# Optimization experiments

Hardware: AMD Instinct MI355X
Metric: run time of the kernel (lower is better)

The kernel has to match this reference:

```python
import jax, jax.numpy as jnp
import numpy as np

N = 50000          # nodes
E = 1600000        # edges (avg degree 32)
NUM_FEAT = 512
HIDDEN = 128
NUM_CLASS = 40
NUM_LAYERS = 4
EPS = 0.3


def setup_inputs() -> dict:
    key = jax.random.key(0)
    ks = jax.random.split(key, 8)
    x = jax.random.normal(ks[0], (N, NUM_FEAT), dtype=jnp.float32)
    edge_index = jax.random.randint(ks[1], (2, E), 0, N, dtype=jnp.int64)
    gain = 1.414  # xavier_normal_(gain=1.414) as in reset_parameters
    W1 = jax.random.normal(ks[2], (HIDDEN, NUM_FEAT), dtype=jnp.float32) * gain * (2.0 / (HIDDEN + NUM_FEAT)) ** 0.5
    b1 = jnp.zeros((HIDDEN,), dtype=jnp.float32)
    W2 = jax.random.normal(ks[3], (NUM_CLASS, HIDDEN), dtype=jnp.float32) * gain * (2.0 / (NUM_CLASS + HIDDEN)) ** 0.5
    b2 = jnp.zeros((NUM_CLASS,), dtype=jnp.float32)
    # FAConv attention vectors: Linear(channels, 1, bias=False) per layer
    att_l = jax.random.normal(ks[4], (NUM_LAYERS, HIDDEN), dtype=jnp.float32) * (2.0 / (1 + HIDDEN)) ** 0.5
    att_r = jax.random.normal(ks[5], (NUM_LAYERS, HIDDEN), dtype=jnp.float32) * (2.0 / (1 + HIDDEN)) ** 0.5
    return dict(x=x, edge_index=edge_index, W1=W1, b1=b1, W2=W2, b2=b2, att_l=att_l, att_r=att_r)


def reference(x, edge_index, W1, b1, W2, b2, att_l, att_r):
    n = x.shape[0]
    # gcn_norm with self-loops (FAConv default add_self_loops=True)
    loops = jnp.arange(n, dtype=edge_index.dtype)
    src = jnp.concatenate([edge_index[0], loops])  # source j
    dst = jnp.concatenate([edge_index[1], loops])  # target i
    deg = jax.ops.segment_sum(jnp.ones_like(src, dtype=x.dtype), dst, num_segments=n)
    dis = jax.lax.rsqrt(jnp.maximum(deg, 1.0))
    norm = dis[src] * dis[dst]  # [E+N]

    # eval mode: dropout is identity
    h = jax.nn.relu(x @ W1.T + b1)  # [N, HIDDEN]
    raw = h
    for l in range(NUM_LAYERS):
        al = h @ att_l[l]  # [N]
        ar = h @ att_r[l]  # [N]
        coef = jnp.tanh(al[src] + ar[dst]) * norm            # [E+N]
        agg = jax.ops.segment_sum(h[src] * coef[:, None], dst, num_segments=n)
        h = agg + EPS * raw
    logits = h @ W2.T + b2  # [N, NUM_CLASS]
    return jax.nn.log_softmax(logits, axis=1)
```

## Files before the change

kernel.cpp:

```cpp
#include <hip/hip_runtime.h>
#include <cmath>


#define HIDDEN 128
#define FEAT 512
#define NCLASS 40
#define LDST 40
#define LDSW 132
#define NB 256
#define PITCH 12544
#define BM1 64

typedef __attribute__((ext_vector_type(8))) short short8;
typedef __attribute__((ext_vector_type(4))) float f32x4;
typedef __attribute__((ext_vector_type(2))) float f32x2;

__device__ __forceinline__ float bf_lo(unsigned u) { return __uint_as_float(u << 16); }
__device__ __forceinline__ float bf_hi(unsigned u) { return __uint_as_float(u & 0xffff0000u); }
__device__ __forceinline__ f32x2 up2(unsigned u) {
    f32x2 v; v.x = bf_lo(u); v.y = bf_hi(u); return v;
}
__device__ __forceinline__ unsigned pack_bf16(float x, float y) {
    unsigned ux = __float_as_uint(x);
    unsigned uy = __float_as_uint(y);
    unsigned lx = (ux + 0x7fffu + ((ux >> 16) & 1u)) >> 16;
    unsigned hy = (uy + 0x7fffu + ((uy >> 16) & 1u)) & 0xffff0000u;
    return hy | lx;
}
__device__ __forceinline__ float fast_tanh(float x) {
    x = fminf(fmaxf(x, -15.f), 15.f);
    float e = __expf(2.f * x);
    return (e - 1.f) / (e + 1.f);
}

#define ACC4P(c, r) { f32x2 c2; c2.x = c; c2.y = c; \
    acc2[0] = __builtin_elementwise_fma(c2, up2(r.x), acc2[0]); \
    acc2[1] = __builtin_elementwise_fma(c2, up2(r.y), acc2[1]); \
    acc2[2] = __builtin_elementwise_fma(c2, up2(r.z), acc2[2]); \
    acc2[3] = __builtin_elementwise_fma(c2, up2(r.w), acc2[3]); }

__global__ __launch_bounds__(256) void k_hist(const int* __restrict__ ei, int E, int CE,
                                              unsigned* __restrict__ partial,
                                              ushort* __restrict__ lrank) {
    __shared__ unsigned lh[PITCH];
    const int b = blockIdx.x, tid = threadIdx.x;
    for (int w = tid; w < PITCH; w += 256) lh[w] = 0;
    __syncthreads();
    int e0 = b * CE, e1 = min(E, e0 + CE);
    for (int e = e0 + tid; e < e1; e += 256) {
        int dst = ei[E + e];
        int sh = (dst & 3) * 8;
        unsigned old = atomicAdd(&lh[dst >> 2], 1u << sh);
        lrank[e] = (ushort)((old >> sh) & 0xffu);
    }
    __syncthreads();
    unsigned* prow = partial + (size_t)b * PITCH;
    for (int w = tid; w < PITCH; w += 256) prow[w] = lh[w];
}

__global__ __launch_bounds__(256) void k_hscan(unsigned* __restrict__ partial,
                                               int* __restrict__ deg,
                                               float* __restrict__ dis, int n) {
    int w = blockIdx.x * 256 + threadIdx.x;
    if (w >= PITCH) return;
    unsigned run = 0;
    size_t idx = w;
    for (int b = 0; b < NB; ++b, idx += PITCH) {
        unsigned v = partial[idx];
        partial[idx] = run;
        run += v;
    }
    int node = 4 * w;
    int d0 = run & 0xffu, d1 = (run >> 8) & 0xffu, d2 = (run >> 16) & 0xffu, d3 = run >> 24;
    if (node < n)     { deg[node]     = d0; dis[node]     = rsqrtf((float)(d0 + 1)); }
    if (node + 1 < n) { deg[node + 1] = d1; dis[node + 1] = rsqrtf((float)(d1 + 1)); }
    if (node + 2 < n) { deg[node + 2] = d2; dis[node + 2] = rsqrtf((float)(d2 + 1)); }
    if (node + 3 < n) { deg[node + 3] = d3; dis[node + 3] = rsqrtf((float)(d3 + 1)); }
}

__global__ __launch_bounds__(256) void k_scan1(const int* __restrict__ deg, int* __restrict__ offs,
                                               int* __restrict__ part, int n) {
    __shared__ int s[256];
    int tid = threadIdx.x;
    int gid = blockIdx.x * 256 + tid;
    int v = (gid < n) ? deg[gid] : 0;
    s[tid] = v;
    __syncthreads();
    for (int off = 1; off < 256; off <<= 1) {
        int t = (tid >= off) ? s[tid - off] : 0;
        __syncthreads();
        s[tid] += t;
        __syncthreads();
    }
    if (gid < n) offs[gid] = s[tid] - v;
    if (tid == 255) part[blockIdx.x] = s[255];
}

__global__ __launch_bounds__(256) void k_scan2(int* __restrict__ part, int nb) {
    __shared__ int s[256];
    int tid = threadIdx.x;
    int v = (tid < nb) ? part[tid] : 0;
    s[tid] = v;
    __syncthreads();
    for (int off = 1; off < 256; off <<= 1) {
        int t = (tid >= off) ? s[tid - off] : 0;
        __syncthreads();
        s[tid] += t;
        __syncthreads();
    }
    if (tid < nb) part[tid] = s[tid] - v;
}

__global__ __launch_bounds__(256) void k_scan3(int* __restrict__ offs, const int* __restrict__ part,
                                               int n, int E) {
    int gid = blockIdx.x * 256 + threadIdx.x;
    if (gid < n) offs[gid] += part[blockIdx.x];
    if (gid == 0) offs[n] = E;
}

__global__ __launch_bounds__(256) void k_csr_fill(const int* __restrict__ ei, int E, int CE,
                                                  const int* __restrict__ offs,
                                                  const unsigned* __restrict__ partial,
                                                  const ushort* __restrict__ lrank,
                                                  int* __restrict__ csrc) {
    __shared__ unsigned lp[PITCH];
    const int b = blockIdx.x, tid = threadIdx.x;
    const unsigned* prow = partial + (size_t)b * PITCH;
    for (int w = tid; w < PITCH; w += 256) lp[w] = prow[w];
    __syncthreads();
    int e0 = b * CE, e1 = min(E, e0 + CE);
    for (int e = e0 + tid; e < e1; e += 256) {
        int dst = ei[E + e];
        int src = ei[e];
        unsigned wv = lp[dst >> 2];
        int base = (wv >> ((dst & 3) * 8)) & 0xffu;
        csrc[offs[dst] + base + (int)lrank[e]] = src;
    }
}

__global__ __launch_bounds__(256) void k_gemm1p(const float* __restrict__ x,
                                                const float* __restrict__ W1,
                                                const float* __restrict__ b1,
                                                float* __restrict__ h,
                                                unsigned* __restrict__ hbf,
                                                const float* __restrict__ attl,
                                                const float* __restrict__ attr,
                                                const float* __restrict__ dis,
                                                float2* __restrict__ al2,
                                                float* __restrict__ ar_out, int M) {
    __shared__ ushort As[BM1 * LDST];
    __shared__ ushort Bs[128 * LDST];
    __shared__ float hs[BM1][HIDDEN + 1];
    const int tid = threadIdx.x;
    const int bm = blockIdx.x * BM1;
    const int wave = tid >> 6, lane = tid & 63;
    const int rh = (wave >> 1) * 32;
    const int ch = (wave & 1) * 64;
    const int sub = lane & 15, quad = lane >> 4;
    const int lrow = tid >> 3;
    const int lcol = (tid & 7) * 4;
    f32x4 acc[2][4] = {};
    float4 av[2], bv[4];
#pragma unroll
    for (int i = 0; i < 2; ++i) {
        int grow = bm + lrow + 32 * i;
        av[i] = (grow < M) ? *(const float4*)(x + (size_t)grow * FEAT + lcol)
                           : make_float4(0.f, 0.f, 0.f, 0.f);
    }
#pragma unroll
    for (int i = 0; i < 4; ++i)
        bv[i] = *(const float4*)(W1 + (size_t)(lrow + 32 * i) * FEAT + lcol);

    for (int k0 = 0; k0 < FEAT; k0 += 32) {
#pragma unroll
        for (int i = 0; i < 2; ++i)
            *(uint2*)(As + (lrow + 32 * i) * LDST + lcol) =
                make_uint2(pack_bf16(av[i].x, av[i].y), pack_bf16(av[i].z, av[i].w));
#pragma unroll
        for (int i = 0; i < 4; ++i)
            *(uint2*)(Bs + (lrow + 32 * i) * LDST + lcol) =
                make_uint2(pack_bf16(bv[i].x, bv[i].y), pack_bf16(bv[i].z, bv[i].w));
        __syncthreads();
        if (k0 + 32 < FEAT) {
            const int kn = k0 + 32;
#pragma unroll
            for (int i = 0; i < 2; ++i) {
                int grow = bm + lrow + 32 * i;
                av[i] = (grow < M) ? *(const float4*)(x + (size_t)grow * FEAT + kn + lcol)
                                   : make_float4(0.f, 0.f, 0.f, 0.f);
            }
#pragma unroll
            for (int i = 0; i < 4; ++i)
                bv[i] = *(const float4*)(W1 + (size_t)(lrow + 32 * i) * FEAT + kn + lcol);
        }
        short8 af[2], bfr[4];
#pragma unroll
        for (int t = 0; t < 2; ++t)
            af[t] = *(const short8*)(As + (rh + t * 16 + sub) * LDST + quad * 8);
#pragma unroll
        for (int u = 0; u < 4; ++u)
            bfr[u] = *(const short8*)(Bs + (ch + u * 16 + sub) * LDST + quad * 8);
#pragma unroll
        for (int t = 0; t < 2; ++t)
#pragma unroll
            for (int u = 0; u < 4; ++u)
                acc[t][u] = __builtin_amdgcn_mfma_f32_16x16x32_bf16(af[t], bfr[u], acc[t][u], 0, 0, 0);
        __syncthreads();
    }
    float b1v[4];
#pragma unroll
    for (int u = 0; u < 4; ++u) b1v[u] = b1[ch + u * 16 + sub];
#pragma unroll
    for (int t = 0; t < 2; ++t) {
#pragma unroll
        for (int u = 0; u < 4; ++u) {
            int col = ch + u * 16 + sub;
#pragma unroll
            for (int r2 = 0; r2 < 4; ++r2) {
                int r = rh + t * 16 + quad * 4 + r2;
                int grow = bm + r;
                float v = fmaxf(acc[t][u][r2] + b1v[u], 0.f);
                hs[r][col] = v;
                if (grow < M)
                    h[(size_t)grow * HIDDEN + col] = v;
            }
        }
    }
    __syncthreads();
    {
        const float al0 = attl[2 * lane], al1 = attl[2 * lane + 1];
        const float ab0 = attr[2 * lane], ab1 = attr[2 * lane + 1];
        for (int i = 0; i < 16; ++i) {
            int ln = wave * 16 + i;
            int node = bm + ln;
            if (node >= M) break;
            float2 hv = *(const float2*)(&hs[ln][2 * lane]);
            hbf[(size_t)node * 64 + lane] = pack_bf16(hv.x, hv.y);
            float pl = hv.x * al0 + hv.y * al1;
            float pr = hv.x * ab0 + hv.y * ab1;
            for (int off = 32; off; off >>= 1) {
                pl += __shfl_down(pl, off);
                pr += __shfl_down(pr, off);
            }
            if (lane == 0) {
                al2[node] = make_float2(pl, dis[node]);
                ar_out[node] = pr;
            }
        }
    }
}

__global__ __launch_bounds__(256) void k_aggregate(
                            const unsigned* __restrict__ hbf, const float* __restrict__ raw,
                            const float2* __restrict__ al2, const float* __restrict__ ar,
                            const int* __restrict__ offs, const int* __restrict__ csrc,
                            float* __restrict__ hout, unsigned* __restrict__ houtbf,
                            const float* __restrict__ attl_n, const float* __restrict__ attr_n,
                            float2* __restrict__ al2_o, float* __restrict__ ar_o, int n) {
    int node = (blockIdx.x * blockDim.x + threadIdx.x) >> 6;
    int lane = threadIdx.x & 63;
    if (node >= n) return;
    const int grp = lane >> 4;
    const int sub = lane & 15;
    const float arn = ar[node];
    const float2 selfld = al2[node];
    const float disn = selfld.y;
    f32x2 acc2[4] = {};
    int e0 = offs[node], e1 = offs[node + 1];
    for (int base = e0; base < e1; base += 64) {
        int cnt = min(64, e1 - base);
        int idx = base + lane;
        int smy = (lane < cnt) ? csrc[idx] : node;
        float2 lmy = al2[smy];
        float cmy = (lane < cnt) ? fast_tanh(lmy.x + arn) * lmy.y * disn : 0.f;
        int t = 0;
        for (; t + 16 <= cnt; t += 16) {
            int sa = __shfl(smy, t + grp);
            int sb = __shfl(smy, t + 4 + grp);
            int sc = __shfl(smy, t + 8 + grp);
            int sd = __shfl(smy, t + 12 + grp);
            float ca = __shfl(cmy, t + grp);
            float cb = __shfl(cmy, t + 4 + grp);
            float cc = __shfl(cmy, t + 8 + grp);
            float cd = __shfl(cmy, t + 12 + grp);
            uint4 ra = *(const uint4*)(hbf + (size_t)sa * 64 + sub * 4);
            uint4 rb = *(const uint4*)(hbf + (size_t)sb * 64 + sub * 4);
            uint4 rc = *(const uint4*)(hbf + (size_t)sc * 64 + sub * 4);
            uint4 rd = *(const uint4*)(hbf + (size_t)sd * 64 + sub * 4);
            ACC4P(ca, ra); ACC4P(cb, rb); ACC4P(cc, rc); ACC4P(cd, rd);
        }
        for (; t < cnt; t += 4) {
            int sa = __shfl(smy, t + grp);
            float ca = __shfl(cmy, t + grp);
            uint4 ra = *(const uint4*)(hbf + (size_t)sa * 64 + sub * 4);
            ACC4P(ca, ra);
        }
    }
#pragma unroll
    for (int j = 0; j < 4; ++j) {
        acc2[j].x += __shfl_xor(acc2[j].x, 16);
        acc2[j].y += __shfl_xor(acc2[j].y, 16);
        acc2[j].x += __shfl_xor(acc2[j].x, 32);
        acc2[j].y += __shfl_xor(acc2[j].y, 32);
    }
    {
        float c = fast_tanh(selfld.x + arn) * disn * disn;
        uint4 r = *(const uint4*)(hbf + (size_t)node * 64 + sub * 4);
        ACC4P(c, r);
    }
    float o[8];
    {
        float4 rv0 = *(const float4*)(raw + (size_t)node * HIDDEN + sub * 8);
        float4 rv1 = *(const float4*)(raw + (size_t)node * HIDDEN + sub * 8 + 4);
        o[0] = acc2[0].x + 0.3f * rv0.x; o[1] = acc2[0].y + 0.3f * rv0.y;
        o[2] = acc2[1].x + 0.3f * rv0.z; o[3] = acc2[1].y + 0.3f * rv0.w;
        o[4] = acc2[2].x + 0.3f * rv1.x; o[5] = acc2[2].y + 0.3f * rv1.y;
        o[6] = acc2[3].x + 0.3f * rv1.z; o[7] = acc2[3].y + 0.3f * rv1.w;
    }
    if (grp == 0) {
        if (hout) {
            *(float4*)(hout + (size_t)node * HIDDEN + sub * 8) = make_float4(o[0], o[1], o[2], o[3]);
            *(float4*)(hout + (size_t)node * HIDDEN + sub * 8 + 4) = make_float4(o[4], o[5], o[6], o[7]);
        }
        if (houtbf) {
            uint4 pk = make_uint4(pack_bf16(o[0], o[1]), pack_bf16(o[2], o[3]),
                                  pack_bf16(o[4], o[5]), pack_bf16(o[6], o[7]));
            *(uint4*)(houtbf + (size_t)node * 64 + sub * 4) = pk;
        }
    }
    if (attl_n) {
        float4 a0 = *(const float4*)(attl_n + sub * 8);
        float4 a1 = *(const float4*)(attl_n + sub * 8 + 4);
        float4 c0 = *(const float4*)(attr_n + sub * 8);
        float4 c1 = *(const float4*)(attr_n + sub * 8 + 4);
        float pl = o[0] * a0.x + o[1] * a0.y + o[2] * a0.z + o[3] * a0.w +
                   o[4] * a1.x + o[5] * a1.y + o[6] * a1.z + o[7] * a1.w;
        float pr = o[0] * c0.x + o[1] * c0.y + o[2] * c0.z + o[3] * c0.w +
                   o[4] * c1.x + o[5] * c1.y + o[6] * c1.z + o[7] * c1.w;
        for (int off = 8; off; off >>= 1) {
            pl += __shfl_xor(pl, off);
            pr += __shfl_xor(pr, off);
        }
        if (lane == 0) {
            al2_o[node] = make_float2(pl, disn);
            ar_o[node] = pr;
        }
    }
}

__global__ __launch_bounds__(256, 4) void k_out(const float* __restrict__ h,
                                                const float* __restrict__ W2,
                                                const float* __restrict__ b2,
                                                float* __restrict__ out, int n) {
    __shared__ float ws[NCLASS * LDSW];
    __shared__ float bs[NCLASS];
    const int tid = threadIdx.x;
    for (int i = tid; i < NCLASS * (HIDDEN / 4); i += 256) {
        int r = i >> 5;
        int c4 = i & 31;
        *(float4*)(ws + r * LDSW + c4 * 4) = ((const float4*)W2)[i];
    }
    if (tid < NCLASS) bs[tid] = b2[tid];
    __syncthreads();
    int node = blockIdx.x * 32 + (tid >> 3);
    const int ol = tid & 7;
    if (node >= n) return;
    const float* hr = h + (size_t)node * HIDDEN;
    float acc[5];
#pragma unroll
    for (int c = 0; c < 5; ++c) acc[c] = bs[ol + 8 * c];
#pragma unroll
    for (int k0 = 0; k0 < HIDDEN; k0 += 16) {
        float4 h0 = *(const float4*)(hr + k0);
        float4 h1 = *(const float4*)(hr + k0 + 4);
        float4 h2v = *(const float4*)(hr + k0 + 8);
        float4 h3 = *(const float4*)(hr + k0 + 12);
#pragma unroll
        for (int c = 0; c < 5; ++c) {
            const float* w = ws + (ol + 8 * c) * LDSW + k0;
            float4 w0 = *(const float4*)(w);
            float4 w1 = *(const float4*)(w + 4);
            float4 w2v = *(const float4*)(w + 8);
            float4 w3 = *(const float4*)(w + 12);
            acc[c] += h0.x * w0.x + h0.y * w0.y + h0.z * w0.z + h0.w * w0.w +
                      h1.x * w1.x + h1.y * w1.y + h1.z * w1.z + h1.w * w1.w +
                      h2v.x * w2v.x + h2v.y * w2v.y + h2v.z * w2v.z + h2v.w * w2v.w +
                      h3.x * w3.x + h3.y * w3.y + h3.z * w3.z + h3.w * w3.w;
        }
    }
    float m = acc[0];
#pragma unroll
    for (int c = 1; c < 5; ++c) m = fmaxf(m, acc[c]);
    m = fmaxf(m, __shfl_xor(m, 1));
    m = fmaxf(m, __shfl_xor(m, 2));
    m = fmaxf(m, __shfl_xor(m, 4));
    float ssum = 0.f;
#pragma unroll
    for (int c = 0; c < 5; ++c) ssum += expf(acc[c] - m);
    ssum += __shfl_xor(ssum, 1);
    ssum += __shfl_xor(ssum, 2);
    ssum += __shfl_xor(ssum, 4);
    float lse = m + logf(ssum);
    float* orow = out + (size_t)node * NCLASS;
#pragma unroll
    for (int c = 0; c < 5; ++c) orow[ol + 8 * c] = acc[c] - lse;
}

extern "C" void kernel_launch(void* const* d_in, const int* in_sizes, int n_in,
                              void* d_out, int out_size, void* d_ws, size_t ws_size,
                              hipStream_t stream) {
    const float* x    = (const float*)d_in[0];
    const int*   ei   = (const int*)d_in[1];
    const float* W1   = (const float*)d_in[2];
    const float* b1   = (const float*)d_in[3];
    const float* W2   = (const float*)d_in[4];
    const float* b2   = (const float*)d_in[5];
    const float* attl = (const float*)d_in[6];
    const float* attr = (const float*)d_in[7];
    const int N = in_sizes[0] / FEAT;
    const int E = in_sizes[1] / 2;
    float* out = (float*)d_out;

    char* p = (char*)d_ws;
    auto take = [&](size_t bytes) {
        void* q = (void*)p;
        p += (bytes + 255) & ~(size_t)255;
        return q;
    };
    float*    h0   = (float*)take((size_t)N * HIDDEN * 4);
    float*    h2   = (float*)take((size_t)N * HIDDEN * 4);
    unsigned* hb0  = (unsigned*)take((size_t)N * 64 * 4);
    unsigned* hb1  = (unsigned*)take((size_t)N * 64 * 4);
    int*      deg  = (int*)take((size_t)N * 4);
    float*    dis  = (float*)take((size_t)N * 4);
    int*      offs = (int*)take((size_t)(N + 1) * 4);
    unsigned* partial = (unsigned*)take((size_t)NB * PITCH * 4);
    ushort*   lrank   = (ushort*)take((size_t)E * 2);
    int*      csrc = (int*)take((size_t)E * 4);
    float2*   al2A = (float2*)take((size_t)N * 8);
    float2*   al2B = (float2*)take((size_t)N * 8);
    float*    arA  = (float*)take((size_t)N * 4);
    float*    arB  = (float*)take((size_t)N * 4);
    int*      part = (int*)take(1024);

    const int nbl = (N + 255) / 256;
    const int CE = (E + NB - 1) / NB;

    k_hist<<<NB, 256, 0, stream>>>(ei, E, CE, partial, lrank);
    k_hscan<<<(PITCH + 255) / 256, 256, 0, stream>>>(partial, deg, dis, N);
    k_scan1<<<nbl, 256, 0, stream>>>(deg, offs, part, N);
    k_scan2<<<1, 256, 0, stream>>>(part, nbl);
    k_scan3<<<nbl, 256, 0, stream>>>(offs, part, N, E);
    k_csr_fill<<<NB, 256, 0, stream>>>(ei, E, CE, offs, partial, lrank, csrc);

    k_gemm1p<<<(N + BM1 - 1) / BM1, 256, 0, stream>>>(x, W1, b1, h0, hb0,
                                                      attl, attr, dis, al2A, arA, N);

    unsigned* hbin = hb0, *hbout = hb1;
    float2*   alin = al2A, *alout = al2B;
    float*    arin = arA,  *arout = arB;
    for (int l = 0; l < 4; ++l) {
        const bool last = (l == 3);
        const float* attl_n = (!last) ? (attl + (l + 1) * HIDDEN) : nullptr;
        const float* attr_n = (!last) ? (attr + (l + 1) * HIDDEN) : nullptr;
        float*    fo  = last ? h2 : nullptr;
        unsigned* hbo = last ? nullptr : hbout;
        k_aggregate<<<(N + 3) / 4, 256, 0, stream>>>(hbin, h0, alin, arin, offs, csrc,
                                                     fo, hbo, attl_n, attr_n,
                                                     alout, arout, N);
        unsigned* tb = hbin; hbin = hbout; hbout = tb;
        float2* ta = alin; alin = alout; alout = ta;
        float* tr = arin; arin = arout; arout = tr;
    }

    k_out<<<(N + 31) / 32, 256, 0, stream>>>(h2, W2, b2, out, N);
}
```

Baseline: 513.7 us.

## Halve GEMM1 row tile and compute attention dots from registers

The first GEMM block tile shrinks from 64 to 32 rows, with each of the four waves now owning a 32-column slice instead of a 2x2 split. The large shared-memory staging buffer for h is removed. The bf16 packing and the att_l/att_r dot products are computed straight from the MFMA accumulator registers using lane shuffles, and a small per-wave partial-sum array is reduced in shared memory. This cuts LDS use and the serial per-node reduction loop and raises block count, at the cost of re-reading W1 twice as often per output row.

```diff
diff --git a/kernel.cpp b/kernel.cpp
--- a/kernel.cpp
+++ b/kernel.cpp
@@ -9,7 +9,7 @@
 #define LDSW 132
 #define NB 256
 #define PITCH 12544
-#define BM1 64
+#define BM1 32
 
 typedef __attribute__((ext_vector_type(8))) short short8;
 typedef __attribute__((ext_vector_type(4))) float f32x4;
@@ -150,32 +150,27 @@
                                                 float* __restrict__ ar_out, int M) {
     __shared__ ushort As[BM1 * LDST];
     __shared__ ushort Bs[128 * LDST];
-    __shared__ float hs[BM1][HIDDEN + 1];
+    __shared__ float pd[4][BM1][2];
     const int tid = threadIdx.x;
     const int bm = blockIdx.x * BM1;
     const int wave = tid >> 6, lane = tid & 63;
-    const int rh = (wave >> 1) * 32;
-    const int ch = (wave & 1) * 64;
+    const int ch = wave * 32;
     const int sub = lane & 15, quad = lane >> 4;
     const int lrow = tid >> 3;
     const int lcol = (tid & 7) * 4;
-    f32x4 acc[2][4] = {};
-    float4 av[2], bv[4];
-#pragma unroll
-    for (int i = 0; i < 2; ++i) {
-        int grow = bm + lrow + 32 * i;
-        av[i] = (grow < M) ? *(const float4*)(x + (size_t)grow * FEAT + lcol)
-                           : make_float4(0.f, 0.f, 0.f, 0.f);
-    }
-#pragma unroll
-    for (int i = 0; i < 4; ++i)
-        bv[i] = *(const float4*)(W1 + (size_t)(lrow + 32 * i) * FEAT + lcol);
-
+    f32x4 acc[2][2] = {};
+    float4 av, bv[4];
+    {
+        int grow = bm + lrow;
+        av = (grow < M) ? *(const float4*)(x + (size_t)grow * FEAT + lcol)
+                        : make_float4(0.f, 0.f, 0.f, 0.f);
+#pragma unroll
+        for (int i = 0; i < 4; ++i)
+            bv[i] = *(const float4*)(W1 + (size_t)(lrow + 32 * i) * FEAT + lcol);
+    }
     for (int k0 = 0; k0 < FEAT; k0 += 32) {
-#pragma unroll
-        for (int i = 0; i < 2; ++i)
-            *(uint2*)(As + (lrow + 32 * i) * LDST + lcol) =
-                make_uint2(pack_bf16(av[i].x, av[i].y), pack_bf16(av[i].z, av[i].w));
+        *(uint2*)(As + lrow * LDST + lcol) =
+            make_uint2(pack_bf16(av.x, av.y), pack_bf16(av.z, av.w));
 #pragma unroll
         for (int i = 0; i < 4; ++i)
             *(uint2*)(Bs + (lrow + 32 * i) * LDST + lcol) =
@@ -183,69 +178,89 @@
         __syncthreads();
         if (k0 + 32 < FEAT) {
             const int kn = k0 + 32;
-#pragma unroll
-            for (int i = 0; i < 2; ++i) {
-                int grow = bm + lrow + 32 * i;
-                av[i] = (grow < M) ? *(const float4*)(x + (size_t)grow * FEAT + kn + lcol)
-                                   : make_float4(0.f, 0.f, 0.f, 0.f);
-            }
+            int grow = bm + lrow;
+            av = (grow < M) ? *(const float4*)(x + (size_t)grow * FEAT + kn + lcol)
+                            : make_float4(0.f, 0.f, 0.f, 0.f);
 #pragma unroll
             for (int i = 0; i < 4; ++i)
                 bv[i] = *(const float4*)(W1 + (size_t)(lrow + 32 * i) * FEAT + kn + lcol);
         }
-        short8 af[2], bfr[4];
+        short8 af[2], bfr[2];
 #pragma unroll
         for (int t = 0; t < 2; ++t)
-            af[t] = *(const short8*)(As + (rh + t * 16 + sub) * LDST + quad * 8);
-#pragma unroll
-        for (int u = 0; u < 4; ++u)
+            af[t] = *(const short8*)(As + (t * 16 + sub) * LDST + quad * 8);
+#pragma unroll
+        for (int u = 0; u < 2; ++u)
             bfr[u] = *(const short8*)(Bs + (ch + u * 16 + sub) * LDST + quad * 8);
 #pragma unroll
         for (int t = 0; t < 2; ++t)
 #pragma unroll
-            for (int u = 0; u < 4; ++u)
+            for (int u = 0; u < 2; ++u)
                 acc[t][u] = __builtin_amdgcn_mfma_f32_16x16x32_bf16(af[t], bfr[u], acc[t][u], 0, 0, 0);
         __syncthreads();
     }
-    float b1v[4];
-#pragma unroll
-    for (int u = 0; u < 4; ++u) b1v[u] = b1[ch + u * 16 + sub];
-#pragma unroll
-    for (int t = 0; t < 2; ++t) {
-#pragma unroll
-        for (int u = 0; u < 4; ++u) {
-            int col = ch + u * 16 + sub;
+    float b1v[2];
+#pragma unroll
+    for (int u = 0; u < 2; ++u) b1v[u] = b1[ch + u * 16 + sub];
+    float v[2][2][4];
+#pragma unroll
+    for (int t = 0; t < 2; ++t)
+#pragma unroll
+        for (int u = 0; u < 2; ++u)
 #pragma unroll
             for (int r2 = 0; r2 < 4; ++r2) {
-                int r = rh + t * 16 + quad * 4 + r2;
+                int r = t * 16 + quad * 4 + r2;
                 int grow = bm + r;
-                float v = fmaxf(acc[t][u][r2] + b1v[u], 0.f);
-                hs[r][col] = v;
+                float vv = fmaxf(acc[t][u][r2] + b1v[u], 0.f);
+                v[t][u][r2] = vv;
                 if (grow < M)
-                    h[(size_t)grow * HIDDEN + col] = v;
+                    h[(size_t)grow * HIDDEN + ch + u * 16 + sub] = vv;
             }
-        }
-    }
-    __syncthreads();
-    {
-        const float al0 = attl[2 * lane], al1 = attl[2 * lane + 1];
-        const float ab0 = attr[2 * lane], ab1 = attr[2 * lane + 1];
-        for (int i = 0; i < 16; ++i) {
-            int ln = wave * 16 + i;
-            int node = bm + ln;
-            if (node >= M) break;
-            float2 hv = *(const float2*)(&hs[ln][2 * lane]);
-            hbf[(size_t)node * 64 + lane] = pack_bf16(hv.x, hv.y);
-            float pl = hv.x * al0 + hv.y * al1;
-            float pr = hv.x * ab0 + hv.y * ab1;
-            for (int off = 32; off; off >>= 1) {
-                pl += __shfl_down(pl, off);
-                pr += __shfl_down(pr, off);
+#pragma unroll
+    for (int t = 0; t < 2; ++t)
+#pragma unroll
+        for (int u = 0; u < 2; ++u)
+#pragma unroll
+            for (int r2 = 0; r2 < 4; ++r2) {
+                float vp = __shfl_xor(v[t][u][r2], 1);
+                if (!(lane & 1)) {
+                    int node = bm + t * 16 + quad * 4 + r2;
+                    if (node < M) {
+                        unsigned pk = pack_bf16(v[t][u][r2], vp);
+                        hbf[(size_t)node * 64 + ((ch + u * 16 + sub) >> 1)] = pk;
+                    }
+                }
             }
-            if (lane == 0) {
-                al2[node] = make_float2(pl, dis[node]);
-                ar_out[node] = pr;
+    float alc[2], arc[2];
+#pragma unroll
+    for (int u = 0; u < 2; ++u) {
+        alc[u] = attl[ch + u * 16 + sub];
+        arc[u] = attr[ch + u * 16 + sub];
+    }
+#pragma unroll
+    for (int t = 0; t < 2; ++t)
+#pragma unroll
+        for (int r2 = 0; r2 < 4; ++r2) {
+            float pl = v[t][0][r2] * alc[0] + v[t][1][r2] * alc[1];
+            float pr = v[t][0][r2] * arc[0] + v[t][1][r2] * arc[1];
+            pl += __shfl_xor(pl, 1); pl += __shfl_xor(pl, 2);
+            pl += __shfl_xor(pl, 4); pl += __shfl_xor(pl, 8);
+            pr += __shfl_xor(pr, 1); pr += __shfl_xor(pr, 2);
+            pr += __shfl_xor(pr, 4); pr += __shfl_xor(pr, 8);
+            if (sub == 0) {
+                int r = t * 16 + quad * 4 + r2;
+                pd[wave][r][0] = pl;
+                pd[wave][r][1] = pr;
             }
+        }
+    __syncthreads();
+    if (tid < BM1) {
+        int node = bm + tid;
+        if (node < M) {
+            float pl = pd[0][tid][0] + pd[1][tid][0] + pd[2][tid][0] + pd[3][tid][0];
+            float pr = pd[0][tid][1] + pd[1][tid][1] + pd[2][tid][1] + pd[3][tid][1];
+            al2[node] = make_float2(pl, dis[node]);
+            ar_out[node] = pr;
         }
     }
 }
```

Result: no change. 510.2 us (-0.7%).
